# Kernel optimization log

Hardware: AMD Instinct MI355X
Metric: run time of the kernel (lower is better)

Reference implementation:

```python
import jax, jax.numpy as jnp
import numpy as np
from jax import lax

B, CIN, H, W = 32, 256, 64, 64
K, STRIDE = 9, 2
CAPS_TYPES, OS0, OS1 = 32, 8, 1
NUM_ITER = 3
OH = (H - K) // STRIDE + 1  # 28
OW = (W - K) // STRIDE + 1  # 28
EPS = 1e-8


def squash(x):
    # Hinton squash over capsule pose dims (os0, os1)
    n2 = jnp.sum(x * x, axis=(-2, -1), keepdims=True)
    return (n2 / (1.0 + n2)) * x / jnp.sqrt(n2 + EPS)


def setup_inputs() -> dict:
    key = jax.random.key(0)
    k1, k2 = jax.random.split(key)
    x = jax.random.normal(k1, (B, CIN, H, W), jnp.float32)
    cout = CAPS_TYPES * OS0 * OS1
    conv_w = jax.random.normal(k2, (cout, CIN, K, K), jnp.float32) / np.float32(np.sqrt(CIN * K * K))
    conv_b = jnp.zeros((cout,), jnp.float32)
    routing_bias = jnp.full((CAPS_TYPES, OH, OW, OS0, OS1), 0.1, jnp.float32)
    return {"x": x, "conv_w": conv_w, "conv_b": conv_b, "routing_bias": routing_bias}


def reference(x, conv_w, conv_b, routing_bias):
    b = x.shape[0]
    caps = lax.conv_general_dilated(
        x, conv_w, (STRIDE, STRIDE), 'VALID',
        dimension_numbers=('NCHW', 'OIHW', 'NCHW'))
    caps = caps + conv_b[None, :, None, None]
    # [b, C*os0*os1, oh, ow] -> [b, C, oh, ow, os0, os1]
    caps = caps.reshape(b, CAPS_TYPES, OS0, OS1, OH, OW).transpose(0, 1, 4, 5, 2, 3)
    poses = squash(caps)
    # Dynamic routing (degenerate: one vote per output capsule, singleton input dims)
    votes = poses  # [b, C, oh, ow, os0, os1]
    logits = jnp.zeros((b, CAPS_TYPES, OH, OW), caps.dtype)
    for _ in range(NUM_ITER):
        c = jax.nn.softmax(logits, axis=1)           # couplings over output caps types
        s = c[..., None, None] * votes + routing_bias  # weighted vote sum (+ bias)
        poses = squash(s)
        logits = logits + jnp.sum(votes * poses, axis=(-2, -1))  # agreement update
    acts = jnp.sqrt(jnp.sum(poses * poses, axis=(-2, -1)))  # [b, C, oh, ow]
    return poses, acts
```

## Files before the change

kernel.cpp:

```cpp
#include <hip/hip_runtime.h>

#define B_    32
#define CIN_  256
#define H_    64
#define W_    64
#define OH_   28
#define OW_   28
#define M_TOTAL 25088
#define POSE_ELEMS 6422528

typedef _Float16 f16;
typedef _Float16 f16x8 __attribute__((ext_vector_type(8)));
typedef _Float16 f16x4 __attribute__((ext_vector_type(4)));
typedef float    f32x4 __attribute__((ext_vector_type(4)));

#define GLD_LDS16(gp, lp) __builtin_amdgcn_global_load_lds( \
    (const __attribute__((address_space(1))) void*)(gp),    \
    (__attribute__((address_space(3))) void*)(lp), 16, 0, 0)

#define SBAR()    asm volatile("s_barrier" ::: "memory")
#define WAITVM0() asm volatile("s_waitcnt vmcnt(0)" ::: "memory")
#define WAITVM4() asm volatile("s_waitcnt vmcnt(4)" ::: "memory")
#define LGKM8()   asm volatile("s_waitcnt lgkmcnt(8)" ::: "memory")

__global__ __launch_bounds__(256) void xt_kernel(const float* __restrict__ x,
                                                 f16* __restrict__ Xt)
{
    __shared__ float tile[64 * 65];
    const int t  = threadIdx.x;
    const int c0 = blockIdx.x * 64;
    const int h  = blockIdx.y;
    const int b  = blockIdx.z;

    const float* src = x + (((long)(b * CIN_ + c0)) * H_ + h) * W_;
    const int ci = t >> 6, w = t & 63;
#pragma unroll
    for (int it = 0; it < 16; ++it) {
        const int c = it * 4 + ci;
        tile[c * 65 + w] = src[(long)c * (H_ * W_) + w];
    }
    __syncthreads();

    f16* dst = Xt + ((long)(b * H_ + h) * W_) * CIN_ + c0;
    const int wq = t >> 4, cq = t & 15;
#pragma unroll
    for (int it = 0; it < 4; ++it) {
        const int w2 = it * 16 + wq;
        f16x4 v;
        v[0] = (f16)tile[(cq * 4 + 0) * 65 + w2];
        v[1] = (f16)tile[(cq * 4 + 1) * 65 + w2];
        v[2] = (f16)tile[(cq * 4 + 2) * 65 + w2];
        v[3] = (f16)tile[(cq * 4 + 3) * 65 + w2];
        *(f16x4*)(dst + (long)w2 * CIN_ + cq * 4) = v;
    }
}

__global__ __launch_bounds__(256) void wt_kernel(const float* __restrict__ w,
                                                 f16* __restrict__ Wt)
{
    __shared__ float tile[64 * 81];
    const int t  = threadIdx.x;
    const int co = blockIdx.x >> 2;
    const int c0 = (blockIdx.x & 3) * 64;
    const float* src = w + ((long)co * 256 + c0) * 81;
    for (int i = t; i < 64 * 81; i += 256) tile[i] = src[i];
    __syncthreads();
    for (int i = t; i < 64 * 81; i += 256) {
        const int khw = i >> 6, ci = i & 63;
        Wt[(long)khw * 65536 + co * 256 + c0 + ci] = (f16)tile[ci * 81 + khw];
    }
}

__global__ __launch_bounds__(512, 2) void gemm_kernel(const f16* __restrict__ Xt,
                                                      const f16* __restrict__ Wt,
                                                      float* __restrict__ part,
                                                      int nsplit)
{
    __shared__ __align__(16) char lds[131072];
    char* ldsA = lds;
    char* ldsB = lds + 65536;

    const int t    = threadIdx.x;
    const int lane = t & 63, wave = t >> 6;

    const int nwg = 98 * nsplit;
    const int q = nwg >> 3, r8 = nwg & 7;
    const int xcd = blockIdx.x & 7, idx = blockIdx.x >> 3;
    const int wgid = (xcd < r8 ? xcd * (q + 1) : r8 * (q + 1) + (xcd - r8) * q) + idx;
    const int sk = wgid / 98;
    const int mt = wgid - sk * 98;
    const int m0 = mt * 256;

    const int ntb = 324 / nsplit, rem = 324 - ntb * nsplit;
    const int ksb = sk * ntb + (sk < rem ? sk : rem);
    const int NT  = ntb + (sk < rem ? 1 : 0);

    const int csrc = ((lane & 7) ^ (lane >> 3)) * 8;
    int aoff[4], boff[4];
#pragma unroll
    for (int i = 0; i < 4; ++i) {
        const int r  = (i * 8 + wave) * 8 + (lane >> 3);
        const int ga = (r & 63) + ((r >> 6) & 1) * 128 + (r >> 7) * 64;
        const int m  = m0 + ga;
        const int b   = m / 784;
        const int rem2 = m - b * 784;
        const int oh  = rem2 / 28;
        const int ow  = rem2 - oh * 28;
        aoff[i] = ((b * 64 + 2 * oh) * 64 + 2 * ow) * 256 + csrc;
        const int gb = (r & 31) + ((r >> 5) & 3) * 64 + (r >> 7) * 32;
        boff[i] = gb * 256 + csrc;
    }

    const int wm = wave >> 2, wn = wave & 3;
    int rowA[8], rowB[4];
#pragma unroll
    for (int mf = 0; mf < 8; ++mf) {
        const int g  = wm * 128 + mf * 16 + (lane & 15);
        const int lr = (g & 63) + ((g >> 6) & 1) * 128 + (g >> 7) * 64;
        rowA[mf] = lr * 128;
    }
#pragma unroll
    for (int nf = 0; nf < 4; ++nf) {
        const int g  = wn * 64 + nf * 16 + (lane & 15);
        const int lr = (g & 31) + ((g >> 6) << 5) + ((g >> 5) & 1) * 128;
        rowB[nf] = lr * 128;
    }
    int csw[2];
    csw[0] = ((lane >> 4) * 16) ^ ((lane & 7) << 4);
    csw[1] = 64 ^ csw[0];

    f32x4 acc[8][4];
    const f32x4 z = {0.f, 0.f, 0.f, 0.f};
#pragma unroll
    for (int i = 0; i < 8; ++i)
#pragma unroll
        for (int j = 0; j < 4; ++j) acc[i][j] = z;

#define KOFFS(KS, AK, BK)                                      \
    {  const int cb_ = (KS) & 3, khw_ = (KS) >> 2;             \
       const int kh_ = khw_ / 9, kw_ = khw_ - kh_ * 9;         \
       AK = (kh_ * 64 + kw_) * 256 + cb_ * 64;                 \
       BK = khw_ * 65536 + cb_ * 64; }

#define STAGE_A_HALF(H, AK, NB) do {                                               \
    GLD_LDS16(Xt + aoff[2*(H)]   + (AK), ldsA + (NB)*32768 + ((2*(H))*8   + wave)*1024); \
    GLD_LDS16(Xt + aoff[2*(H)+1] + (AK), ldsA + (NB)*32768 + ((2*(H)+1)*8 + wave)*1024); } while(0)
#define STAGE_B_HALF(H, BK, NB) do {                                               \
    GLD_LDS16(Wt + boff[2*(H)]   + (BK), ldsB + (NB)*32768 + ((2*(H))*8   + wave)*1024); \
    GLD_LDS16(Wt + boff[2*(H)+1] + (BK), ldsB + (NB)*32768 + ((2*(H)+1)*8 + wave)*1024); } while(0)

#define MFMA_PAIR(MI, NI, A, Bf)                                                        \
    acc[MI][NI] = __builtin_amdgcn_mfma_f32_16x16x32_f16((A)[0], (Bf)[0], acc[MI][NI], 0,0,0); \
    acc[MI][NI] = __builtin_amdgcn_mfma_f32_16x16x32_f16((A)[1], (Bf)[1], acc[MI][NI], 0,0,0);
#define MFMA_Q(MH, NH, BF)                                          \
    MFMA_PAIR((MH)*4+0, (NH)*2+0, af[0], BF[0]) MFMA_PAIR((MH)*4+0, (NH)*2+1, af[0], BF[1]) \
    MFMA_PAIR((MH)*4+1, (NH)*2+0, af[1], BF[0]) MFMA_PAIR((MH)*4+1, (NH)*2+1, af[1], BF[1]) \
    MFMA_PAIR((MH)*4+2, (NH)*2+0, af[2], BF[0]) MFMA_PAIR((MH)*4+2, (NH)*2+1, af[2], BF[1]) \
    MFMA_PAIR((MH)*4+3, (NH)*2+0, af[3], BF[0]) MFMA_PAIR((MH)*4+3, (NH)*2+1, af[3], BF[1])

#define READ_AF(P, MH) do {                                           \
    _Pragma("unroll")                                                 \
    for (int k_ = 0; k_ < 4; ++k_) {                                  \
        af[k_][0] = *(const f16x8*)((P) + rowA[(MH)*4+k_] + csw[0]);  \
        af[k_][1] = *(const f16x8*)((P) + rowA[(MH)*4+k_] + csw[1]);  \
    } } while(0)
#define READ_BF(P, V, NH) do {                                        \
    _Pragma("unroll")                                                 \
    for (int k_ = 0; k_ < 2; ++k_) {                                  \
        V[k_][0] = *(const f16x8*)((P) + rowB[(NH)*2+k_] + csw[0]);   \
        V[k_][1] = *(const f16x8*)((P) + rowB[(NH)*2+k_] + csw[1]);   \
    } } while(0)

    f16x8 af[4][2], bf0[2][2], bf1[2][2];

    {
        int ak0, bk0;
        KOFFS(ksb, ak0, bk0);
        STAGE_A_HALF(0, ak0, 0);
        STAGE_B_HALF(0, bk0, 0);
        STAGE_B_HALF(1, bk0, 0);
        STAGE_A_HALF(1, ak0, 0);
    }
    WAITVM4();
    SBAR();

#pragma unroll 1
    for (int tt = 0; tt < NT; ++tt) {
        const int c = tt & 1, nc = c ^ 1;
        const int ksn = ksb + ((tt + 1 < NT) ? tt + 1 : tt);
        int akn, bkn;
        KOFFS(ksn, akn, bkn);
        const char* pA = ldsA + c * 32768;
        const char* pB = ldsB + c * 32768;

        STAGE_A_HALF(0, akn, nc);
        WAITVM4();
        READ_AF(pA, 0);
        READ_BF(pB, bf0, 0);
        LGKM8();
        SBAR();
        __builtin_amdgcn_s_setprio(1);
        MFMA_Q(0, 0, bf0)
        __builtin_amdgcn_s_setprio(0);

        STAGE_B_HALF(0, bkn, nc);
        WAITVM4();
        READ_BF(pB, bf1, 1);
        SBAR();
        __builtin_amdgcn_s_setprio(1);
        MFMA_Q(0, 1, bf1)
        __builtin_amdgcn_s_setprio(0);

        STAGE_B_HALF(1, bkn, nc);
        READ_AF(pA, 1);
        SBAR();
        __builtin_amdgcn_s_setprio(1);
        MFMA_Q(1, 1, bf1)
        __builtin_amdgcn_s_setprio(0);

        STAGE_A_HALF(1, akn, nc);
        WAITVM4();
        SBAR();
        __builtin_amdgcn_s_setprio(1);
        MFMA_Q(1, 0, bf0)
        __builtin_amdgcn_s_setprio(0);
    }
    WAITVM0();

    float* base = part + (long)sk * (M_TOTAL * 256);
    const int lrow = (lane >> 4) * 4;
#pragma unroll
    for (int nf = 0; nf < 4; ++nf) {
        const int n = wn * 64 + nf * 16 + (lane & 15);
#pragma unroll
        for (int mf = 0; mf < 8; ++mf) {
            const long mrow = m0 + wm * 128 + mf * 16 + lrow;
            float* cw = base + mrow * 256 + n;
#pragma unroll
            for (int j = 0; j < 4; ++j) cw[(long)j * 256] = acc[mf][nf][j];
        }
    }
}

__global__ __launch_bounds__(256) void routing_kernel(const float* __restrict__ part,
                                                      const float* __restrict__ bias,
                                                      const float* __restrict__ rb,
                                                      float* __restrict__ out, int nsplit)
{
    const int t   = threadIdx.x;
    const int m   = blockIdx.x * 8 + (t >> 5);
    const int cap = t & 31;
    const int b   = m / 784;
    const int rem = m - b * 784;
    const int oh  = rem / 28;
    const int ow  = rem - oh * 28;

    const float4 b0 = ((const float4*)(bias + cap * 8))[0];
    const float4 b1 = ((const float4*)(bias + cap * 8))[1];
    float v[8] = {b0.x, b0.y, b0.z, b0.w, b1.x, b1.y, b1.z, b1.w};
#pragma unroll 1
    for (int sk = 0; sk < nsplit; ++sk) {
        const float4* cp = (const float4*)(part + (long)sk * (M_TOTAL * 256) + (long)m * 256 + cap * 8);
        const float4 u0 = cp[0], u1 = cp[1];
        v[0] += u0.x; v[1] += u0.y; v[2] += u0.z; v[3] += u0.w;
        v[4] += u1.x; v[5] += u1.y; v[6] += u1.z; v[7] += u1.w;
    }

    float n2 = 0.f;
#pragma unroll
    for (int j = 0; j < 8; ++j) n2 += v[j] * v[j];
    const float f = (n2 / (1.f + n2)) / sqrtf(n2 + 1e-8f);
    float votes[8];
#pragma unroll
    for (int j = 0; j < 8; ++j) votes[j] = f * v[j];

    const float4* rp = (const float4*)(rb + ((long)(cap * 28 + oh) * 28 + ow) * 8);
    const float4 r0 = rp[0], r1 = rp[1];
    const float rbv[8] = {r0.x, r0.y, r0.z, r0.w, r1.x, r1.y, r1.z, r1.w};

    float logit = 0.f;
    float poses[8];
#pragma unroll 1
    for (int it = 0; it < 3; ++it) {
        float mx = logit;
#pragma unroll
        for (int d = 16; d > 0; d >>= 1) mx = fmaxf(mx, __shfl_xor(mx, d, 32));
        const float e = __expf(logit - mx);
        float se = e;
#pragma unroll
        for (int d = 16; d > 0; d >>= 1) se += __shfl_xor(se, d, 32);
        const float c = e / se;

        float s[8];
        float sn2 = 0.f;
#pragma unroll
        for (int j = 0; j < 8; ++j) { s[j] = c * votes[j] + rbv[j]; sn2 += s[j] * s[j]; }
        const float sf = (sn2 / (1.f + sn2)) / sqrtf(sn2 + 1e-8f);
        float dot = 0.f;
#pragma unroll
        for (int j = 0; j < 8; ++j) { poses[j] = sf * s[j]; dot += votes[j] * poses[j]; }
        logit += dot;
    }

    float pn2 = 0.f;
#pragma unroll
    for (int j = 0; j < 8; ++j) pn2 += poses[j] * poses[j];
    const float act = sqrtf(pn2);

    float* po = out + (((long)(b * 32 + cap) * 28 + oh) * 28 + ow) * 8;
    float4 o0 = {poses[0], poses[1], poses[2], poses[3]};
    float4 o1 = {poses[4], poses[5], poses[6], poses[7]};
    ((float4*)po)[0] = o0;
    ((float4*)po)[1] = o1;
    out[POSE_ELEMS + ((long)(b * 32 + cap) * 28 + oh) * 28 + ow] = act;
}

extern "C" void kernel_launch(void* const* d_in, const int* in_sizes, int n_in,
                              void* d_out, int out_size, void* d_ws, size_t ws_size,
                              hipStream_t stream)
{
    const float* x      = (const float*)d_in[0];
    const float* conv_w = (const float*)d_in[1];
    const float* conv_b = (const float*)d_in[2];
    const float* rb     = (const float*)d_in[3];
    float* out          = (float*)d_out;

    char* ws = (char*)d_ws;
    f16*   Xt   = (f16*)ws;
    f16*   Wt   = (f16*)(ws + 67108864);
    const size_t base = 67108864 + 10616832;
    float* part = (float*)(ws + base);
    const size_t part_bytes = (size_t)M_TOTAL * 256 * 4;

    int nsplit = 1;
    if      (ws_size >= base + 5 * part_bytes) nsplit = 5;
    else if (ws_size >= base + 4 * part_bytes) nsplit = 4;
    else if (ws_size >= base + 2 * part_bytes) nsplit = 2;

    xt_kernel<<<dim3(4, 64, 32), 256, 0, stream>>>(x, Xt);
    wt_kernel<<<dim3(1024), 256, 0, stream>>>(conv_w, Wt);
    gemm_kernel<<<dim3(98 * nsplit), dim3(512), 0, stream>>>(Xt, Wt, part, nsplit);
    routing_kernel<<<dim3(3136), 256, 0, stream>>>(part, conv_b, rb, out, nsplit);
}
```

Before: 298.1 us.

## Store split-K partials in fp16 and vectorize input transpose loads

The GEMM now writes its split-K partial sums as fp16 instead of fp32, and the routing kernel reads them as 8-wide half vectors. This halves the partial-buffer write and read traffic. It may also let more splits fit in the workspace, since the size check now uses a smaller partial buffer. Separately, the x transpose kernel loads float4 vectors per thread instead of scalars. Rounding partials to fp16 before summation loses some accuracy.

```diff
diff --git a/kernel.cpp b/kernel.cpp
--- a/kernel.cpp
+++ b/kernel.cpp
@@ -33,11 +33,16 @@
     const int b  = blockIdx.z;
 
     const float* src = x + (((long)(b * CIN_ + c0)) * H_ + h) * W_;
-    const int ci = t >> 6, w = t & 63;
-#pragma unroll
-    for (int it = 0; it < 16; ++it) {
-        const int c = it * 4 + ci;
-        tile[c * 65 + w] = src[(long)c * (H_ * W_) + w];
+    const int w4 = (t & 15) * 4;
+    const int cr = t >> 4;
+#pragma unroll
+    for (int it = 0; it < 4; ++it) {
+        const int c = it * 16 + cr;
+        const float4 v = *(const float4*)(src + (long)c * (H_ * W_) + w4);
+        tile[c * 65 + w4 + 0] = v.x;
+        tile[c * 65 + w4 + 1] = v.y;
+        tile[c * 65 + w4 + 2] = v.z;
+        tile[c * 65 + w4 + 3] = v.w;
     }
     __syncthreads();
 
@@ -73,7 +78,7 @@
 
 __global__ __launch_bounds__(512, 2) void gemm_kernel(const f16* __restrict__ Xt,
                                                       const f16* __restrict__ Wt,
-                                                      float* __restrict__ part,
+                                                      f16* __restrict__ part,
                                                       int nsplit)
 {
     __shared__ __align__(16) char lds[131072];
@@ -227,7 +232,7 @@
     }
     WAITVM0();
 
-    float* base = part + (long)sk * (M_TOTAL * 256);
+    f16* base = part + (long)sk * (M_TOTAL * 256);
     const int lrow = (lane >> 4) * 4;
 #pragma unroll
     for (int nf = 0; nf < 4; ++nf) {
@@ -235,14 +240,14 @@
 #pragma unroll
         for (int mf = 0; mf < 8; ++mf) {
             const long mrow = m0 + wm * 128 + mf * 16 + lrow;
-            float* cw = base + mrow * 256 + n;
-#pragma unroll
-            for (int j = 0; j < 4; ++j) cw[(long)j * 256] = acc[mf][nf][j];
+            f16* cw = base + mrow * 256 + n;
+#pragma unroll
+            for (int j = 0; j < 4; ++j) cw[(long)j * 256] = (f16)acc[mf][nf][j];
         }
     }
 }
 
-__global__ __launch_bounds__(256) void routing_kernel(const float* __restrict__ part,
+__global__ __launch_bounds__(256) void routing_kernel(const f16* __restrict__ part,
                                                       const float* __restrict__ bias,
                                                       const float* __restrict__ rb,
                                                       float* __restrict__ out, int nsplit)
@@ -260,10 +265,9 @@
     float v[8] = {b0.x, b0.y, b0.z, b0.w, b1.x, b1.y, b1.z, b1.w};
 #pragma unroll 1
     for (int sk = 0; sk < nsplit; ++sk) {
-        const float4* cp = (const float4*)(part + (long)sk * (M_TOTAL * 256) + (long)m * 256 + cap * 8);
-        const float4 u0 = cp[0], u1 = cp[1];
-        v[0] += u0.x; v[1] += u0.y; v[2] += u0.z; v[3] += u0.w;
-        v[4] += u1.x; v[5] += u1.y; v[6] += u1.z; v[7] += u1.w;
+        const f16x8 u = *(const f16x8*)(part + (long)sk * (M_TOTAL * 256) + (long)m * 256 + cap * 8);
+#pragma unroll
+        for (int j = 0; j < 8; ++j) v[j] += (float)u[j];
     }
 
     float n2 = 0.f;
@@ -329,8 +333,8 @@
     f16*   Xt   = (f16*)ws;
     f16*   Wt   = (f16*)(ws + 67108864);
     const size_t base = 67108864 + 10616832;
-    float* part = (float*)(ws + base);
-    const size_t part_bytes = (size_t)M_TOTAL * 256 * 4;
+    f16* part = (f16*)(ws + base);
+    const size_t part_bytes = (size_t)M_TOTAL * 256 * 2;
 
     int nsplit = 1;
     if      (ws_size >= base + 5 * part_bytes) nsplit = 5;
```

After: 292.6 us. About the same (-1.8%).
